# Optimization experiments

Hardware: AMD Instinct MI355X
Metric: run time of the kernel (lower is better)

The kernel has to match this reference:

```python
import jax, jax.numpy as jnp
import numpy as np

B, S, E = 2, 2048, 1024
H = 16
D = E // H
LAYER_IDX = 2.0
MASKED_BIAS = -10000.0


def setup_inputs() -> dict:
    key = jax.random.key(0)
    k1, k2, k3 = jax.random.split(key, 3)
    hidden_state = jax.random.normal(k1, (B, S, E), dtype=jnp.float32)
    w_attn = jax.random.normal(k2, (E, 3 * E), dtype=jnp.float32) * 0.2
    b_attn = jnp.zeros((3 * E,), dtype=jnp.float32)
    w_proj = jax.random.normal(k3, (E, E), dtype=jnp.float32) * 0.2
    b_proj = jnp.zeros((E,), dtype=jnp.float32)
    return {"hidden_state": hidden_state, "w_attn": w_attn, "b_attn": b_attn,
            "w_proj": w_proj, "b_proj": b_proj}


def reference(hidden_state, w_attn, b_attn, w_proj, b_proj):
    b, s, e = hidden_state.shape
    # c_attn: Conv1D == x @ W + b, then split into q, k, v
    qkv = hidden_state @ w_attn + b_attn          # [b, s, 3E]
    q, k, v = jnp.split(qkv, 3, axis=-1)
    # split heads -> [b, H, s, D]
    def split_heads(t):
        return t.reshape(b, s, H, D).transpose(0, 2, 1, 3)
    q, k, v = split_heads(q), split_heads(k), split_heads(v)
    # QK^T scaled by sqrt(d_head) then by layer_idx
    scores = jnp.einsum("bhqd,bhkd->bhqk", q, k)
    scores = scores / jnp.asarray(D ** 0.5, scores.dtype)
    scores = scores / LAYER_IDX
    # causal mask with masked_bias fill (-10000.0), matching bias buffer slice
    causal = jnp.tril(jnp.ones((s, s), dtype=bool))  # [s, s]
    scores = jnp.where(causal[None, None, :, :], scores, jnp.asarray(MASKED_BIAS, scores.dtype))
    attn = jax.nn.softmax(scores, axis=-1)
    out = jnp.einsum("bhqk,bhkd->bhqd", attn, v)   # [b, H, s, D]
    # merge heads
    out = out.transpose(0, 2, 1, 3).reshape(b, s, e)
    # c_proj
    return out @ w_proj + b_proj
```

## Files before the change

### kernel.cpp

```cpp
#include <hip/hip_runtime.h>
#include <cstddef>
#include <cstdint>

#define B_DIM   2
#define S_LEN   2048
#define EMB     1024
#define NH      16
#define HD      64
#define QKV_N   3072
#define MROWS   (B_DIM * S_LEN)

using half8  = __attribute__((ext_vector_type(8))) _Float16;
using half4  = __attribute__((ext_vector_type(4))) _Float16;
using f32x4  = __attribute__((ext_vector_type(4))) float;

#if defined(__has_builtin)
#if __has_builtin(__builtin_amdgcn_global_load_lds)
#define HAS_GLL 1
#endif
#endif

__device__ __forceinline__ void stage16(const _Float16* g, _Float16* lds_base, int lane)
{
#ifdef HAS_GLL
    (void)lane;
    __builtin_amdgcn_global_load_lds(
        (const __attribute__((address_space(1))) unsigned int*)g,
        (__attribute__((address_space(3))) unsigned int*)lds_base, 16, 0, 0);
#else
    *(half8*)(lds_base + lane * 8) = *(const half8*)g;
#endif
}

__global__ __launch_bounds__(256)
void prep_all(const float* __restrict__ hidden, const float* __restrict__ w_attn,
              const float* __restrict__ w_proj, _Float16* __restrict__ hidden_h,
              _Float16* __restrict__ wattn_t, _Float16* __restrict__ wproj_t)
{
    const int bid = blockIdx.x, t = threadIdx.x;
    if (bid < 4096) {
        int i = bid * 1024 + t * 4;
        float4 v = *(const float4*)(hidden + i);
        half4 h = { (_Float16)v.x, (_Float16)v.y, (_Float16)v.z, (_Float16)v.w };
        *(half4*)(hidden_h + i) = h;
        return;
    }
    __shared__ float T[32][33];
    const float* W; _Float16* Wt; int N, bx, by;
    if (bid < 7168) {
        int t2 = bid - 4096; bx = t2 % 96; by = t2 / 96; W = w_attn; Wt = wattn_t; N = QKV_N;
    } else {
        int t3 = bid - 7168; bx = t3 & 31; by = t3 >> 5; W = w_proj; Wt = wproj_t; N = EMB;
    }
    const int n0 = bx * 32, k0 = by * 32;
    const int r = t >> 3, c4 = (t & 7) * 4;
    float4 w = *(const float4*)(W + (size_t)(k0 + r) * N + n0 + c4);
    T[r][c4 + 0] = w.x; T[r][c4 + 1] = w.y;
    T[r][c4 + 2] = w.z; T[r][c4 + 3] = w.w;
    __syncthreads();
    half4 h = { (_Float16)T[c4 + 0][r], (_Float16)T[c4 + 1][r],
                (_Float16)T[c4 + 2][r], (_Float16)T[c4 + 3][r] };
    *(half4*)(Wt + (size_t)(n0 + r) * EMB + k0 + c4) = h;
}

template <int MT, int MINW, bool OUT_F16, bool FUSE_VT>
__global__ __launch_bounds__(256, MINW)
void hgemm_lds(const _Float16* __restrict__ X, const _Float16* __restrict__ Wt,
               const float* __restrict__ bias, void* __restrict__ Cout,
               _Float16* __restrict__ vt, int M, int N, int K)
{
    constexpr int BM = MT * 32;
    constexpr int ACALLS = BM / 32;
    __shared__ _Float16 As[BM][64];
    __shared__ _Float16 Bs[128][64];

    const int tid  = threadIdx.x;
    const int wave = tid >> 6, lane = tid & 63;
    const int quad = lane >> 4, l15 = lane & 15;
    const int wm = (wave >> 1) * (MT * 16);
    const int wn = (wave & 1) * 64;
    const int m0 = blockIdx.y * BM, n0 = blockIdx.x * 128;

    const int srow = lane >> 3;
    const int scol = ((lane & 7) ^ srow) * 8;

    const _Float16* xg[ACALLS];
#pragma unroll
    for (int c = 0; c < ACALLS; ++c)
        xg[c] = X + (size_t)(m0 + wave * (BM / 4) + c * 8 + srow) * K + scol;
    const _Float16* wg[4];
#pragma unroll
    for (int c = 0; c < 4; ++c)
        wg[c] = Wt + (size_t)(n0 + wave * 32 + c * 8 + srow) * K + scol;

    f32x4 acc[MT][4] = {};
    const int sx = l15 & 7;

    for (int k0 = 0; k0 < K; k0 += 64) {
#pragma unroll
        for (int c = 0; c < ACALLS; ++c)
            stage16(xg[c] + k0, &As[wave * (BM / 4) + c * 8][0], lane);
#pragma unroll
        for (int c = 0; c < 4; ++c)
            stage16(wg[c] + k0, &Bs[wave * 32 + c * 8][0], lane);
        __syncthreads();

#pragma unroll
        for (int cc = 0; cc < 2; ++cc) {
            half8 af[MT], bf[4];
#pragma unroll
            for (int mt = 0; mt < MT; ++mt)
                af[mt] = *(const half8*)&As[wm + mt * 16 + l15][(((cc * 4 + quad) ^ sx)) * 8];
#pragma unroll
            for (int nt = 0; nt < 4; ++nt)
                bf[nt] = *(const half8*)&Bs[wn + nt * 16 + l15][(((cc * 4 + quad) ^ sx)) * 8];
#pragma unroll
            for (int mt = 0; mt < MT; ++mt)
#pragma unroll
                for (int nt = 0; nt < 4; ++nt)
                    acc[mt][nt] = __builtin_amdgcn_mfma_f32_16x16x32_f16(
                        af[mt], bf[nt], acc[mt][nt], 0, 0, 0);
        }
        __syncthreads();
    }

    if (FUSE_VT && n0 >= 2 * EMB) {
#pragma unroll
        for (int nt = 0; nt < 4; ++nt) {
            const int c  = n0 + wn + nt * 16 + l15;
            const float bv = bias[c];
            const int vcol = c - 2 * EMB;
            const int hh = vcol >> 6, dd = vcol & 63;
#pragma unroll
            for (int mt = 0; mt < MT; ++mt) {
                const int r = m0 + wm + mt * 16 + quad * 4;
                const int bb = r >> 11, ss = r & 2047;
                half4 o = { (_Float16)(acc[mt][nt][0] + bv), (_Float16)(acc[mt][nt][1] + bv),
                            (_Float16)(acc[mt][nt][2] + bv), (_Float16)(acc[mt][nt][3] + bv) };
                *(half4*)(vt + ((size_t)(bb * NH + hh) * HD + dd) * S_LEN + ss) = o;
            }
        }
        return;
    }

#pragma unroll
    for (int nt = 0; nt < 4; ++nt) {
        const int c = n0 + wn + nt * 16 + l15;
        const float bv = bias[c];
#pragma unroll
        for (int mt = 0; mt < MT; ++mt)
#pragma unroll
            for (int reg = 0; reg < 4; ++reg) {
                const int r = m0 + wm + mt * 16 + quad * 4 + reg;
                const float v = acc[mt][nt][reg] + bv;
                if (OUT_F16)
                    ((_Float16*)Cout)[(size_t)r * N + c] = (_Float16)v;
                else
                    ((float*)Cout)[(size_t)r * N + c] = v;
            }
    }
}

__global__ __launch_bounds__(256, 2)
void attn_fa_mfma7(const _Float16* __restrict__ qkv,
                   const _Float16* __restrict__ vt,
                   _Float16* __restrict__ outh)
{
    __shared__ _Float16 Ks[128][64];
    __shared__ _Float16 Vs[64][128];

    const int n   = blockIdx.x;
    const int xcd = n & 7, g = (n >> 3) & 3, j = n >> 5;
    const int bh  = xcd * 4 + g;
    const int qta = j, qtb = 31 - j;
    const int b = bh >> 4, h = bh & 15;

    const int tid  = threadIdx.x;
    const int wave = tid >> 6, lane = tid & 63;
    const int quad = lane >> 4, l15 = lane & 15;
    const size_t row0 = (size_t)b * S_LEN;

    const _Float16 qscale = (_Float16)0.0901684400555602f;
    half8 qfa[2], qfb[2];
    {
        const _Float16* qpa = qkv + (row0 + qta * 64 + wave * 16 + l15) * QKV_N + h * HD + quad * 8;
        const _Float16* qpb = qkv + (row0 + qtb * 64 + wave * 16 + l15) * QKV_N + h * HD + quad * 8;
#pragma unroll
        for (int c = 0; c < 2; ++c) {
            half8 qa = *(const half8*)(qpa + c * 32);
            half8 qb = *(const half8*)(qpb + c * 32);
#pragma unroll
            for (int j2 = 0; j2 < 8; ++j2) { qa[j2] *= qscale; qb[j2] *= qscale; }
            qfa[c] = qa; qfb[c] = qb;
        }
    }

    f32x4 o_a[4] = {}, o_b[4] = {};
    float m_a = -1e30f, l_a = 0.0f, m_b = -1e30f, l_b = 0.0f;

    const int ksrow = lane >> 3;
    const int kscol = ((lane & 7) ^ ksrow) * 8;
    const int vsrow = lane >> 4;
    const _Float16* vbase = vt + (size_t)bh * HD * S_LEN;
    const int sxk = l15 & 7;

    auto softmax_pack = [&](f32x4 (&st)[8], half4 (&pf)[8], float& m_i, float& l_i,
                            f32x4 (&o_acc)[4]) {
        float rm = fmaxf(fmaxf(st[0][0], st[0][1]), fmaxf(st[0][2], st[0][3]));
#pragma unroll
        for (int nt = 1; nt < 8; ++nt) {
            rm = fmaxf(rm, fmaxf(st[nt][0], st[nt][1]));
            rm = fmaxf(rm, fmaxf(st[nt][2], st[nt][3]));
        }
        rm = fmaxf(rm, __shfl_xor(rm, 16));
        rm = fmaxf(rm, __shfl_xor(rm, 32));
        const float mnew = fmaxf(m_i, rm);
        if (__ballot(mnew > m_i)) {
            const float alpha = __builtin_amdgcn_exp2f(m_i - mnew);
            l_i *= alpha;
#pragma unroll
            for (int dt = 0; dt < 4; ++dt)
#pragma unroll
                for (int reg = 0; reg < 4; ++reg) o_acc[dt][reg] *= alpha;
        }
        m_i = mnew;
        float rs = 0.0f;
#pragma unroll
        for (int nt = 0; nt < 8; ++nt) {
            float p0 = __builtin_amdgcn_exp2f(st[nt][0] - mnew);
            float p1 = __builtin_amdgcn_exp2f(st[nt][1] - mnew);
            float p2 = __builtin_amdgcn_exp2f(st[nt][2] - mnew);
            float p3 = __builtin_amdgcn_exp2f(st[nt][3] - mnew);
            rs += (p0 + p1) + (p2 + p3);
            pf[nt] = half4{ (_Float16)p0, (_Float16)p1, (_Float16)p2, (_Float16)p3 };
        }
        rs += __shfl_xor(rs, 16);
        rs += __shfl_xor(rs, 32);
        l_i += rs;
    };

    const int ktNa = (qta + 2) >> 1;
    const int ktNb = (qtb + 2) >> 1;

    for (int kt = 0; kt < ktNb; ++kt) {
        __syncthreads();
        {
            const _Float16* kbase = qkv + (row0 + kt * 128) * QKV_N + EMB + h * HD;
#pragma unroll
            for (int c = 0; c < 4; ++c) {
                const int r0 = wave * 32 + c * 8;
                stage16(kbase + (size_t)(r0 + ksrow) * QKV_N + kscol, &Ks[r0][0], lane);
            }
#pragma unroll
            for (int c = 0; c < 4; ++c) {
                const int r0 = wave * 16 + c * 4;
                const int sgv = ((lane & 15) ^ (c * 4 + vsrow)) * 8;
                stage16(vbase + (size_t)(r0 + vsrow) * S_LEN + kt * 128 + sgv, &Vs[r0][0], lane);
            }
        }
        __syncthreads();

        if (kt < ktNa) {
            f32x4 sa[8] = {}, sb[8] = {};
#pragma unroll
            for (int c = 0; c < 2; ++c)
#pragma unroll
                for (int nt = 0; nt < 8; ++nt) {
                    half8 kf = *(const half8*)&Ks[nt * 16 + l15][((c * 4 + quad) ^ sxk) * 8];
                    sa[nt] = __builtin_amdgcn_mfma_f32_16x16x32_f16(kf, qfa[c], sa[nt], 0, 0, 0);
                    sb[nt] = __builtin_amdgcn_mfma_f32_16x16x32_f16(kf, qfb[c], sb[nt], 0, 0, 0);
                }
            if (kt == ktNa - 1) {
                const int q = qta * 64 + wave * 16 + l15;
#pragma unroll
                for (int nt = 0; nt < 8; ++nt) {
                    const int ks = kt * 128 + nt * 16 + quad * 4;
#pragma unroll
                    for (int reg = 0; reg < 4; ++reg)
                        if (ks + reg > q) sa[nt][reg] = -1e30f;
                }
            }
            half4 pfa[8], pfb[8];
            softmax_pack(sa, pfa, m_a, l_a, o_a);
            softmax_pack(sb, pfb, m_b, l_b, o_b);
#pragma unroll
            for (int nt = 0; nt < 8; ++nt)
#pragma unroll
                for (int dt = 0; dt < 4; ++dt) {
                    const int pg = ((2 * nt + (quad >> 1)) ^ l15) * 8 + (quad & 1) * 4;
                    half4 vf = *(const half4*)&Vs[dt * 16 + l15][pg];
                    o_a[dt] = __builtin_amdgcn_mfma_f32_16x16x16f16(vf, pfa[nt], o_a[dt], 0, 0, 0);
                    o_b[dt] = __builtin_amdgcn_mfma_f32_16x16x16f16(vf, pfb[nt], o_b[dt], 0, 0, 0);
                }
        } else {
            f32x4 sb[8] = {};
#pragma unroll
            for (int c = 0; c < 2; ++c)
#pragma unroll
                for (int nt = 0; nt < 8; ++nt) {
                    half8 kf = *(const half8*)&Ks[nt * 16 + l15][((c * 4 + quad) ^ sxk) * 8];
                    sb[nt] = __builtin_amdgcn_mfma_f32_16x16x32_f16(kf, qfb[c], sb[nt], 0, 0, 0);
                }
            if (kt == ktNb - 1) {
                const int q = qtb * 64 + wave * 16 + l15;
#pragma unroll
                for (int nt = 0; nt < 8; ++nt) {
                    const int ks = kt * 128 + nt * 16 + quad * 4;
#pragma unroll
                    for (int reg = 0; reg < 4; ++reg)
                        if (ks + reg > q) sb[nt][reg] = -1e30f;
                }
            }
            half4 pfb[8];
            softmax_pack(sb, pfb, m_b, l_b, o_b);
#pragma unroll
            for (int nt = 0; nt < 8; ++nt)
#pragma unroll
                for (int dt = 0; dt < 4; ++dt) {
                    const int pg = ((2 * nt + (quad >> 1)) ^ l15) * 8 + (quad & 1) * 4;
                    half4 vf = *(const half4*)&Vs[dt * 16 + l15][pg];
                    o_b[dt] = __builtin_amdgcn_mfma_f32_16x16x16f16(vf, pfb[nt], o_b[dt], 0, 0, 0);
                }
        }
    }

    {
        const float inv = 1.0f / l_a;
        const size_t r = row0 + qta * 64 + wave * 16 + l15;
#pragma unroll
        for (int dt = 0; dt < 4; ++dt) {
            half4 o = { (_Float16)(o_a[dt][0] * inv), (_Float16)(o_a[dt][1] * inv),
                        (_Float16)(o_a[dt][2] * inv), (_Float16)(o_a[dt][3] * inv) };
            *(half4*)(outh + r * EMB + h * HD + dt * 16 + quad * 4) = o;
        }
    }
    {
        const float inv = 1.0f / l_b;
        const size_t r = row0 + qtb * 64 + wave * 16 + l15;
#pragma unroll
        for (int dt = 0; dt < 4; ++dt) {
            half4 o = { (_Float16)(o_b[dt][0] * inv), (_Float16)(o_b[dt][1] * inv),
                        (_Float16)(o_b[dt][2] * inv), (_Float16)(o_b[dt][3] * inv) };
            *(half4*)(outh + r * EMB + h * HD + dt * 16 + quad * 4) = o;
        }
    }
}

extern "C" void kernel_launch(void* const* d_in, const int* in_sizes, int n_in,
                              void* d_out, int out_size, void* d_ws, size_t ws_size,
                              hipStream_t stream)
{
    const float* hidden = (const float*)d_in[0];
    const float* w_attn = (const float*)d_in[1];
    const float* b_attn = (const float*)d_in[2];
    const float* w_proj = (const float*)d_in[3];
    const float* b_proj = (const float*)d_in[4];

    _Float16* hidden_h = (_Float16*)d_ws;
    _Float16* wattn_t  = hidden_h + (size_t)MROWS * EMB;
    _Float16* wproj_t  = wattn_t + (size_t)EMB * QKV_N;
    _Float16* qkv_h    = wproj_t + (size_t)EMB * EMB;
    _Float16* attn_h   = qkv_h + (size_t)MROWS * QKV_N;
    _Float16* vt       = attn_h + (size_t)MROWS * EMB;

    prep_all<<<8192, 256, 0, stream>>>(hidden, w_attn, w_proj,
                                       hidden_h, wattn_t, wproj_t);

    hgemm_lds<4, 3, true, true><<<dim3(QKV_N / 128, MROWS / 128), 256, 0, stream>>>(
        hidden_h, wattn_t, b_attn, qkv_h, vt, MROWS, QKV_N, EMB);

    attn_fa_mfma7<<<dim3(512), 256, 0, stream>>>(qkv_h, vt, attn_h);

    hgemm_lds<2, 4, false, false><<<dim3(EMB / 128, MROWS / 64), 256, 0, stream>>>(
        attn_h, wproj_t, b_proj, d_out, nullptr, MROWS, EMB, EMB);
}
```

Baseline: 172.7 us.

## Fuse hidden fp32-to-fp16 conversion into QKV GEMM and split attention KV across wave groups

Result: slower. 253.6 us (+46.8%).

```diff
diff --git a/kernel.cpp b/kernel.cpp
--- a/kernel.cpp
+++ b/kernel.cpp
@@ -33,24 +33,16 @@
 }
 
 __global__ __launch_bounds__(256)
-void prep_all(const float* __restrict__ hidden, const float* __restrict__ w_attn,
-              const float* __restrict__ w_proj, _Float16* __restrict__ hidden_h,
-              _Float16* __restrict__ wattn_t, _Float16* __restrict__ wproj_t)
+void prep_w(const float* __restrict__ w_attn, const float* __restrict__ w_proj,
+            _Float16* __restrict__ wattn_t, _Float16* __restrict__ wproj_t)
 {
     const int bid = blockIdx.x, t = threadIdx.x;
-    if (bid < 4096) {
-        int i = bid * 1024 + t * 4;
-        float4 v = *(const float4*)(hidden + i);
-        half4 h = { (_Float16)v.x, (_Float16)v.y, (_Float16)v.z, (_Float16)v.w };
-        *(half4*)(hidden_h + i) = h;
-        return;
-    }
     __shared__ float T[32][33];
     const float* W; _Float16* Wt; int N, bx, by;
-    if (bid < 7168) {
-        int t2 = bid - 4096; bx = t2 % 96; by = t2 / 96; W = w_attn; Wt = wattn_t; N = QKV_N;
+    if (bid < 3072) {
+        bx = bid % 96; by = bid / 96; W = w_attn; Wt = wattn_t; N = QKV_N;
     } else {
-        int t3 = bid - 7168; bx = t3 & 31; by = t3 >> 5; W = w_proj; Wt = wproj_t; N = EMB;
+        int t3 = bid - 3072; bx = t3 & 31; by = t3 >> 5; W = w_proj; Wt = wproj_t; N = EMB;
     }
     const int n0 = bx * 32, k0 = by * 32;
     const int r = t >> 3, c4 = (t & 7) * 4;
@@ -63,9 +55,9 @@
     *(half4*)(Wt + (size_t)(n0 + r) * EMB + k0 + c4) = h;
 }
 
-template <int MT, int MINW, bool OUT_F16, bool FUSE_VT>
+template <int MT, int MINW, bool OUT_F16, bool FUSE_VT, bool A_F32>
 __global__ __launch_bounds__(256, MINW)
-void hgemm_lds(const _Float16* __restrict__ X, const _Float16* __restrict__ Wt,
+void hgemm_lds(const void* __restrict__ Xv, const _Float16* __restrict__ Wt,
                const float* __restrict__ bias, void* __restrict__ Cout,
                _Float16* __restrict__ vt, int M, int N, int K)
 {
@@ -85,9 +77,15 @@
     const int scol = ((lane & 7) ^ srow) * 8;
 
     const _Float16* xg[ACALLS];
-#pragma unroll
-    for (int c = 0; c < ACALLS; ++c)
-        xg[c] = X + (size_t)(m0 + wave * (BM / 4) + c * 8 + srow) * K + scol;
+    if (!A_F32) {
+        const _Float16* X = (const _Float16*)Xv;
+#pragma unroll
+        for (int c = 0; c < ACALLS; ++c)
+            xg[c] = X + (size_t)(m0 + wave * (BM / 4) + c * 8 + srow) * K + scol;
+    }
+    const float* Xf = (const float*)Xv;
+    const int ar = tid >> 1, akh = (tid & 1) * 32;
+
     const _Float16* wg[4];
 #pragma unroll
     for (int c = 0; c < 4; ++c)
@@ -97,9 +95,25 @@
     const int sx = l15 & 7;
 
     for (int k0 = 0; k0 < K; k0 += 64) {
-#pragma unroll
-        for (int c = 0; c < ACALLS; ++c)
-            stage16(xg[c] + k0, &As[wave * (BM / 4) + c * 8][0], lane);
+        if (A_F32) {
+            const float* src = Xf + (size_t)(m0 + ar) * K + k0 + akh;
+            float4 f[8];
+#pragma unroll
+            for (int i = 0; i < 8; ++i) f[i] = *(const float4*)(src + i * 4);
+#pragma unroll
+            for (int g2 = 0; g2 < 4; ++g2) {
+                half8 hh = { (_Float16)f[2 * g2].x, (_Float16)f[2 * g2].y,
+                             (_Float16)f[2 * g2].z, (_Float16)f[2 * g2].w,
+                             (_Float16)f[2 * g2 + 1].x, (_Float16)f[2 * g2 + 1].y,
+                             (_Float16)f[2 * g2 + 1].z, (_Float16)f[2 * g2 + 1].w };
+                const int g = (tid & 1) * 4 + g2;
+                *(half8*)&As[ar][(g ^ (ar & 7)) * 8] = hh;
+            }
+        } else {
+#pragma unroll
+            for (int c = 0; c < ACALLS; ++c)
+                stage16(xg[c] + k0, &As[wave * (BM / 4) + c * 8][0], lane);
+        }
 #pragma unroll
         for (int c = 0; c < 4; ++c)
             stage16(wg[c] + k0, &Bs[wave * 32 + c * 8][0], lane);
@@ -161,30 +175,33 @@
     }
 }
 
-__global__ __launch_bounds__(256, 2)
-void attn_fa_mfma7(const _Float16* __restrict__ qkv,
+__global__ __launch_bounds__(512, 4)
+void attn_fa_mfma8(const _Float16* __restrict__ qkv,
                    const _Float16* __restrict__ vt,
                    _Float16* __restrict__ outh)
 {
-    __shared__ _Float16 Ks[128][64];
-    __shared__ _Float16 Vs[64][128];
+    __shared__ _Float16 smem[32768];
 
     const int n   = blockIdx.x;
-    const int xcd = n & 7, g = (n >> 3) & 3, j = n >> 5;
-    const int bh  = xcd * 4 + g;
+    const int xcd = n & 7, g4 = (n >> 3) & 3, j = n >> 5;
+    const int bh  = xcd * 4 + g4;
     const int qta = j, qtb = 31 - j;
     const int b = bh >> 4, h = bh & 15;
 
     const int tid  = threadIdx.x;
     const int wave = tid >> 6, lane = tid & 63;
+    const int grp  = wave >> 2, wl = wave & 3;
     const int quad = lane >> 4, l15 = lane & 15;
     const size_t row0 = (size_t)b * S_LEN;
+
+    _Float16 (*Ks)[64]  = (_Float16(*)[64]) (smem + grp * 8192);
+    _Float16 (*Vs)[128] = (_Float16(*)[128])(smem + 16384 + grp * 8192);
 
     const _Float16 qscale = (_Float16)0.0901684400555602f;
     half8 qfa[2], qfb[2];
     {
-        const _Float16* qpa = qkv + (row0 + qta * 64 + wave * 16 + l15) * QKV_N + h * HD + quad * 8;
-        const _Float16* qpb = qkv + (row0 + qtb * 64 + wave * 16 + l15) * QKV_N + h * HD + quad * 8;
+        const _Float16* qpa = qkv + (row0 + qta * 64 + wl * 16 + l15) * QKV_N + h * HD + quad * 8;
+        const _Float16* qpb = qkv + (row0 + qtb * 64 + wl * 16 + l15) * QKV_N + h * HD + quad * 8;
 #pragma unroll
         for (int c = 0; c < 2; ++c) {
             half8 qa = *(const half8*)(qpa + c * 32);
@@ -241,24 +258,28 @@
 
     const int ktNa = (qta + 2) >> 1;
     const int ktNb = (qtb + 2) >> 1;
-
-    for (int kt = 0; kt < ktNb; ++kt) {
+    const int TMAX = (ktNb + 1) >> 1;
+
+    for (int i = 0; i < TMAX; ++i) {
+        const int kt = grp + 2 * i;
+        const bool valid = kt < ktNb;
         __syncthreads();
-        {
+        if (valid) {
             const _Float16* kbase = qkv + (row0 + kt * 128) * QKV_N + EMB + h * HD;
 #pragma unroll
             for (int c = 0; c < 4; ++c) {
-                const int r0 = wave * 32 + c * 8;
+                const int r0 = wl * 32 + c * 8;
                 stage16(kbase + (size_t)(r0 + ksrow) * QKV_N + kscol, &Ks[r0][0], lane);
             }
 #pragma unroll
             for (int c = 0; c < 4; ++c) {
-                const int r0 = wave * 16 + c * 4;
+                const int r0 = wl * 16 + c * 4;
                 const int sgv = ((lane & 15) ^ (c * 4 + vsrow)) * 8;
                 stage16(vbase + (size_t)(r0 + vsrow) * S_LEN + kt * 128 + sgv, &Vs[r0][0], lane);
             }
         }
         __syncthreads();
+        if (!valid) continue;
 
         if (kt < ktNa) {
             f32x4 sa[8] = {}, sb[8] = {};
@@ -271,7 +292,7 @@
                     sb[nt] = __builtin_amdgcn_mfma_f32_16x16x32_f16(kf, qfb[c], sb[nt], 0, 0, 0);
                 }
             if (kt == ktNa - 1) {
-                const int q = qta * 64 + wave * 16 + l15;
+                const int q = qta * 64 + wl * 16 + l15;
 #pragma unroll
                 for (int nt = 0; nt < 8; ++nt) {
                     const int ks = kt * 128 + nt * 16 + quad * 4;
@@ -302,7 +323,7 @@
                     sb[nt] = __builtin_amdgcn_mfma_f32_16x16x32_f16(kf, qfb[c], sb[nt], 0, 0, 0);
                 }
             if (kt == ktNb - 1) {
-                const int q = qtb * 64 + wave * 16 + l15;
+                const int q = qtb * 64 + wl * 16 + l15;
 #pragma unroll
                 for (int nt = 0; nt < 8; ++nt) {
                     const int ks = kt * 128 + nt * 16 + quad * 4;
@@ -324,24 +345,53 @@
         }
     }
 
-    {
-        const float inv = 1.0f / l_a;
-        const size_t r = row0 + qta * 64 + wave * 16 + l15;
-#pragma unroll
-        for (int dt = 0; dt < 4; ++dt) {
-            half4 o = { (_Float16)(o_a[dt][0] * inv), (_Float16)(o_a[dt][1] * inv),
-                        (_Float16)(o_a[dt][2] * inv), (_Float16)(o_a[dt][3] * inv) };
-            *(half4*)(outh + r * EMB + h * HD + dt * 16 + quad * 4) = o;
-        }
-    }
-    {
-        const float inv = 1.0f / l_b;
-        const size_t r = row0 + qtb * 64 + wave * 16 + l15;
-#pragma unroll
-        for (int dt = 0; dt < 4; ++dt) {
-            half4 o = { (_Float16)(o_b[dt][0] * inv), (_Float16)(o_b[dt][1] * inv),
-                        (_Float16)(o_b[dt][2] * inv), (_Float16)(o_b[dt][3] * inv) };
-            *(half4*)(outh + r * EMB + h * HD + dt * 16 + quad * 4) = o;
+    float* mb = (float*)smem;
+    const int gl = tid & 255;
+    __syncthreads();
+    if (grp == 1) {
+        float* p = mb + gl * 40;
+#pragma unroll
+        for (int dt = 0; dt < 4; ++dt) { *(f32x4*)(p + dt * 4)      = o_a[dt]; }
+#pragma unroll
+        for (int dt = 0; dt < 4; ++dt) { *(f32x4*)(p + 16 + dt * 4) = o_b[dt]; }
+        p[32] = m_a; p[33] = l_a; p[34] = m_b; p[35] = l_b;
+    }
+    __syncthreads();
+    if (grp == 0) {
+        const float* p = mb + gl * 40;
+        {
+            const float m1 = p[32], l1 = p[33];
+            const float m = fmaxf(m_a, m1);
+            const float a0 = __builtin_amdgcn_exp2f(m_a - m);
+            const float a1 = __builtin_amdgcn_exp2f(m1 - m);
+            const float inv = 1.0f / (l_a * a0 + l1 * a1);
+            const size_t r = row0 + qta * 64 + wl * 16 + l15;
+#pragma unroll
+            for (int dt = 0; dt < 4; ++dt) {
+                f32x4 o1 = *(const f32x4*)(p + dt * 4);
+                half4 o = { (_Float16)((o_a[dt][0] * a0 + o1[0] * a1) * inv),
+                            (_Float16)((o_a[dt][1] * a0 + o1[1] * a1) * inv),
+                            (_Float16)((o_a[dt][2] * a0 + o1[2] * a1) * inv),
+                            (_Float16)((o_a[dt][3] * a0 + o1[3] * a1) * inv) };
+                *(half4*)(outh + r * EMB + h * HD + dt * 16 + quad * 4) = o;
+            }
+        }
+        {
+            const float m1 = p[34], l1 = p[35];
+            const float m = fmaxf(m_b, m1);
+            const float a0 = __builtin_amdgcn_exp2f(m_b - m);
+            const float a1 = __builtin_amdgcn_exp2f(m1 - m);
+            const float inv = 1.0f / (l_b * a0 + l1 * a1);
+            const size_t r = row0 + qtb * 64 + wl * 16 + l15;
+#pragma unroll
+            for (int dt = 0; dt < 4; ++dt) {
+                f32x4 o1 = *(const f32x4*)(p + 16 + dt * 4);
+                half4 o = { (_Float16)((o_b[dt][0] * a0 + o1[0] * a1) * inv),
+                            (_Float16)((o_b[dt][1] * a0 + o1[1] * a1) * inv),
+                            (_Float16)((o_b[dt][2] * a0 + o1[2] * a1) * inv),
+                            (_Float16)((o_b[dt][3] * a0 + o1[3] * a1) * inv) };
+                *(half4*)(outh + r * EMB + h * HD + dt * 16 + quad * 4) = o;
+            }
         }
     }
 }
@@ -356,21 +406,19 @@
     const float* w_proj = (const float*)d_in[3];
     const float* b_proj = (const float*)d_in[4];
 
-    _Float16* hidden_h = (_Float16*)d_ws;
-    _Float16* wattn_t  = hidden_h + (size_t)MROWS * EMB;
-    _Float16* wproj_t  = wattn_t + (size_t)EMB * QKV_N;
-    _Float16* qkv_h    = wproj_t + (size_t)EMB * EMB;
-    _Float16* attn_h   = qkv_h + (size_t)MROWS * QKV_N;
-    _Float16* vt       = attn_h + (size_t)MROWS * EMB;
-
-    prep_all<<<8192, 256, 0, stream>>>(hidden, w_attn, w_proj,
-                                       hidden_h, wattn_t, wproj_t);
-
-    hgemm_lds<4, 3, true, true><<<dim3(QKV_N / 128, MROWS / 128), 256, 0, stream>>>(
-        hidden_h, wattn_t, b_attn, qkv_h, vt, MROWS, QKV_N, EMB);
-
-    attn_fa_mfma7<<<dim3(512), 256, 0, stream>>>(qkv_h, vt, attn_h);
-
-    hgemm_lds<2, 4, false, false><<<dim3(EMB / 128, MROWS / 64), 256, 0, stream>>>(
+    _Float16* wattn_t = (_Float16*)d_ws;
+    _Float16* wproj_t = wattn_t + (size_t)EMB * QKV_N;
+    _Float16* qkv_h   = wproj_t + (size_t)EMB * EMB;
+    _Float16* attn_h  = qkv_h + (size_t)MROWS * QKV_N;
+    _Float16* vt      = attn_h + (size_t)MROWS * EMB;
+
+    prep_w<<<4096, 256, 0, stream>>>(w_attn, w_proj, wattn_t, wproj_t);
+
+    hgemm_lds<4, 3, true, true, true><<<dim3(QKV_N / 128, MROWS / 128), 256, 0, stream>>>(
+        hidden, wattn_t, b_attn, qkv_h, vt, MROWS, QKV_N, EMB);
+
+    attn_fa_mfma8<<<dim3(512), 512, 0, stream>>>(qkv_h, vt, attn_h);
+
+    hgemm_lds<2, 4, false, false, false><<<dim3(EMB / 128, MROWS / 64), 256, 0, stream>>>(
         attn_h, wproj_t, b_proj, d_out, nullptr, MROWS, EMB, EMB);
 }
```
